# Performance work log

Hardware: AMD Instinct MI355X
Metric: run time of the kernel (lower is better)

## Reference

```python
import jax, jax.numpy as jnp
import numpy as np

THRESH = 0.999  # dynamic outlier percentile

# Standard NF4 signpost values (normalized to [-1, 1])
NF4 = np.array([-1.0, -0.6961928009986877, -0.5250730514526367, -0.39491748809814453,
                -0.28444138169288635, -0.18477343022823334, -0.09105003625154495, 0.0,
                0.07958029955625534, 0.16093020141124725, 0.24611230194568634, 0.33791524171829224,
                0.44070982933044434, 0.5626170039176941, 0.7229568362236023, 1.0], dtype=np.float32)


def setup_inputs() -> dict:
    key = jax.random.key(0)
    k1, k2 = jax.random.split(key)
    x = jax.random.normal(k1, (4096, 4096), dtype=jnp.float32)        # [tokens, in_features]
    weight = jax.random.normal(k2, (4096, 4096), dtype=jnp.float32)   # [out_features, in_features]
    nf_lut = jnp.asarray(NF4)                                          # [16] NF4 poles
    return {"x": x, "weight": weight, "nf_lut": nf_lut}


def quantize_nf(weight, nf_lut):
    # --- dynamic outlier detection (get_outliers_dynamic, qchannel=-1) ---
    t = 1.0 - (1.0 - THRESH) / 2.0
    upper = jnp.quantile(weight, t, axis=-1, keepdims=True)        # [R,1]
    lower = jnp.quantile(weight, 1.0 - t, axis=-1, keepdims=True)  # [R,1]
    outlier_mask = (weight <= lower) | (weight >= upper)           # [R,C] bool

    # --- include_sparse scale computation (quant_fn_nf) ---
    outliers0 = weight * outlier_mask
    median = jnp.median(weight, axis=-1, keepdims=True)
    tmp = weight - outliers0 + median * outlier_mask               # outliers replaced by median
    maxval = jnp.max(tmp, axis=-1, keepdims=True)
    minval = jnp.min(tmp, axis=-1, keepdims=True)
    offset = (maxval + minval) * 0.5
    rangeval = (maxval - minval) * 0.5

    w = weight - offset
    outliers = w * outlier_mask        # sparse (fp) component
    w = w - outliers                   # dense component
    w_scaled = w / rangeval            # normalized to ~[-1, 1]

    # --- nearest-pole (NF) rounding: argmin over |w - pole| ---
    idx = jnp.argmin(jnp.abs(w_scaled[..., None] - nf_lut), axis=-1)  # [R,C]
    Q = nf_lut[idx].astype(jnp.float16).astype(jnp.float32)           # .half() in torch

    # --- dequant ---
    qw = Q * rangeval + outliers + offset
    qw = jnp.nan_to_num(qw, nan=0.0, posinf=0.0, neginf=0.0)
    return qw


def reference(x, weight, nf_lut):
    qweight = quantize_nf(weight, nf_lut)   # simulated NF4 dense+sparse dequant
    return x @ qweight.T                    # [tokens, out_features]
```

## Files before the change

kernel.cpp:

```cpp
#include <hip/hip_runtime.h>
#include <hip/hip_fp16.h>
#include <stdint.h>

typedef __attribute__((ext_vector_type(4))) float f32x4;
typedef __attribute__((ext_vector_type(8))) short short8;

__device__ __forceinline__ unsigned short f2bf(float f) {
  unsigned int b = __float_as_uint(f);
  b = b + 0x7FFFu + ((b >> 16) & 1u);
  return (unsigned short)(b >> 16);
}

#define CE(a, b) { float _lo = fminf((a), (b)), _hi = fmaxf((a), (b)); (a) = _lo; (b) = _hi; }

__device__ __forceinline__ void merge8(float x[8]) {
  CE(x[0], x[4]); CE(x[1], x[5]); CE(x[2], x[6]); CE(x[3], x[7]);
  CE(x[2], x[4]); CE(x[3], x[5]);
  CE(x[1], x[2]); CE(x[3], x[4]); CE(x[5], x[6]);
}

__global__ __launch_bounds__(256) void prep_kernel(const float* __restrict__ x,
                                                   const float* __restrict__ W,
                                                   const float* __restrict__ lut,
                                                   unsigned short* __restrict__ xb,
                                                   unsigned short* __restrict__ qb) {
  const int tid = threadIdx.x;

  if (blockIdx.x >= 4096) {
    int b = blockIdx.x - 4096;
    int base = b * 1024 + tid;
#pragma unroll
    for (int it = 0; it < 4; ++it) {
      int i = base + it * 256;
      f32x4 v = ((const f32x4*)x)[i];
      ushort4 u;
      u.x = f2bf(v[0]); u.y = f2bf(v[1]); u.z = f2bf(v[2]); u.w = f2bf(v[3]);
      ((ushort4*)xb)[i] = u;
    }
    return;
  }

  const int C = 4096;
  const int row = blockIdx.x;
  const int lane = tid & 63;
  const int wv = tid >> 6;

  __shared__ float s_luth[16];
  __shared__ float s_mid[15];
  __shared__ float s_red[4][8];
  __shared__ float s_par[4];

  if (tid < 16) {
    float f = lut[tid];
    s_luth[tid] = __half2float(__float2half(f));
  }
  if (tid < 15) s_mid[tid] = 0.5f * (lut[tid] + lut[tid + 1]);

  const f32x4* Wp = (const f32x4*)(W + (size_t)row * C);
  f32x4 v[4];
#pragma unroll
  for (int i = 0; i < 4; ++i) v[i] = Wp[i * 256 + tid];

  float bot[4] = {__builtin_inff(), __builtin_inff(), __builtin_inff(), __builtin_inff()};
  float top[4] = {-__builtin_inff(), -__builtin_inff(), -__builtin_inff(), -__builtin_inff()};
#pragma unroll
  for (int i = 0; i < 4; ++i) {
#pragma unroll
    for (int j = 0; j < 4; ++j) {
      float f = v[i][j];
      bot[3] = fminf(bot[3], f); CE(bot[2], bot[3]); CE(bot[1], bot[2]); CE(bot[0], bot[1]);
      top[0] = fmaxf(top[0], f); CE(top[0], top[1]); CE(top[1], top[2]); CE(top[2], top[3]);
    }
  }

#pragma unroll
  for (int d = 1; d < 64; d <<= 1) {
    float xx[8];
#pragma unroll
    for (int j = 0; j < 4; ++j) { xx[j] = bot[j]; xx[4 + j] = __shfl_xor(bot[j], d); }
    merge8(xx);
#pragma unroll
    for (int j = 0; j < 4; ++j) bot[j] = xx[j];
#pragma unroll
    for (int j = 0; j < 4; ++j) { xx[j] = top[j]; xx[4 + j] = __shfl_xor(top[j], d); }
    merge8(xx);
#pragma unroll
    for (int j = 0; j < 4; ++j) top[j] = xx[4 + j];
  }

  if (lane == 0) {
#pragma unroll
    for (int j = 0; j < 4; ++j) { s_red[wv][j] = bot[j]; s_red[wv][4 + j] = top[j]; }
  }
  __syncthreads();

  if (tid == 0) {
    float a[8], b[8], m[8];
#pragma unroll
    for (int j = 0; j < 4; ++j) { a[j] = s_red[0][j]; a[4 + j] = s_red[1][j]; }
    merge8(a);
#pragma unroll
    for (int j = 0; j < 4; ++j) { b[j] = s_red[2][j]; b[4 + j] = s_red[3][j]; }
    merge8(b);
#pragma unroll
    for (int j = 0; j < 4; ++j) { m[j] = a[j]; m[4 + j] = b[j]; }
    merge8(m);
    float lower = m[2] + 0.0475f * (m[3] - m[2]);
#pragma unroll
    for (int j = 0; j < 4; ++j) { a[j] = s_red[0][4 + j]; a[4 + j] = s_red[1][4 + j]; }
    merge8(a);
#pragma unroll
    for (int j = 0; j < 4; ++j) { b[j] = s_red[2][4 + j]; b[4 + j] = s_red[3][4 + j]; }
    merge8(b);
#pragma unroll
    for (int j = 0; j < 4; ++j) { m[j] = a[4 + j]; m[4 + j] = b[4 + j]; }
    merge8(m);
    float upper = m[4] + 0.9525f * (m[5] - m[4]);
    s_par[0] = lower; s_par[1] = upper;
  }
  __syncthreads();

  float lower = s_par[0], upper = s_par[1];

  float mn = __builtin_inff(), mx = -__builtin_inff();
#pragma unroll
  for (int i = 0; i < 4; ++i) {
#pragma unroll
    for (int j = 0; j < 4; ++j) {
      float f = v[i][j];
      bool outl = (f <= lower) || (f >= upper);
      if (!outl) { mn = fminf(mn, f); mx = fmaxf(mx, f); }
    }
  }
#pragma unroll
  for (int d = 1; d < 64; d <<= 1) {
    mn = fminf(mn, __shfl_xor(mn, d));
    mx = fmaxf(mx, __shfl_xor(mx, d));
  }
  if (lane == 0) { s_red[wv][0] = mn; s_red[wv][1] = mx; }
  __syncthreads();
  if (tid == 0) {
    float tmn = fminf(fminf(s_red[0][0], s_red[1][0]), fminf(s_red[2][0], s_red[3][0]));
    float tmx = fmaxf(fmaxf(s_red[0][1], s_red[1][1]), fmaxf(s_red[2][1], s_red[3][1]));
    s_par[2] = (tmx + tmn) * 0.5f;
    s_par[3] = (tmx - tmn) * 0.5f;
  }
  __syncthreads();
  float offset = s_par[2], range = s_par[3];
  float invr = 1.0f / range;

  unsigned short* outr = qb + (size_t)row * C;
#pragma unroll
  for (int i = 0; i < 4; ++i) {
    ushort4 o;
    unsigned short os[4];
#pragma unroll
    for (int j = 0; j < 4; ++j) {
      float f = v[i][j];
      bool outl = (f <= lower) || (f >= upper);
      float q;
      if (outl) {
        q = f;
      } else {
        float ws = (f - offset) * invr;
        int bi = (ws > s_mid[7]) ? 8 : 0;
        bi += (ws > s_mid[bi + 3]) ? 4 : 0;
        bi += (ws > s_mid[bi + 1]) ? 2 : 0;
        bi += (ws > s_mid[bi]) ? 1 : 0;
        q = s_luth[bi] * range + offset;
      }
      if (!isfinite(q)) q = 0.0f;
      os[j] = f2bf(q);
    }
    o.x = os[0]; o.y = os[1]; o.z = os[2]; o.w = os[3];
    ((ushort4*)outr)[i * 256 + tid] = o;
  }
}

#define GK 4096

__device__ __forceinline__ void gload16(const void* gp, void* lp) {
  __builtin_amdgcn_global_load_lds(
      (const __attribute__((address_space(1))) unsigned int*)(uintptr_t)gp,
      (__attribute__((address_space(3))) unsigned int*)(unsigned int)(uintptr_t)lp,
      16, 0, 0);
}

#define BAR()    __builtin_amdgcn_s_barrier()
#define LGKM0()  asm volatile("s_waitcnt lgkmcnt(0)" ::: "memory")
#define VM6()    asm volatile("s_waitcnt vmcnt(6)" ::: "memory")
#define PRIO1()  __builtin_amdgcn_s_setprio(1)
#define PRIO0()  __builtin_amdgcn_s_setprio(0)

__global__ __launch_bounds__(512, 2) void gemm_bt(const unsigned short* __restrict__ A,
                                                  const unsigned short* __restrict__ B,
                                                  float* __restrict__ C) {
  __shared__ __align__(16) unsigned short sA[2][2][8192];
  __shared__ __align__(16) unsigned short sB[2][2][8192];

  const int tid = threadIdx.x;
  const int lane = tid & 63;
  const int wv = tid >> 6;
  const int wm = wv >> 2, wn = wv & 3;
  const int fr = lane & 15, fk = lane >> 4;

  int bi = blockIdx.x;
  int swz = (bi & 7) * 32 + (bi >> 3);
  int brow = swz >> 4, bcol = swz & 15;

  const unsigned short* Abase = A + (size_t)brow * 256 * GK;
  const unsigned short* Bbase = B + (size_t)bcol * 256 * GK;

  const int cA = (fk * 16) ^ ((fr & 8) << 2);

  const int srow = (wv >> 1) * 16 + (lane >> 2);
  const int skelt = ((wv & 1) * 64 + (((lane & 3) * 16) ^ ((lane & 32) ? 32 : 0))) >> 1;

  auto stage = [&](const unsigned short* gb, unsigned short* lb, int h, int kt) {
    const unsigned short* g = gb + ((size_t)h * 128) * GK + kt * 64 + skelt;
    char* lc = (char*)lb + wv * 1024 + lane * 16;
#pragma unroll
    for (int l = 0; l < 2; ++l)
      gload16(g + (size_t)(l * 64 + srow) * GK, lc + l * 8192);
  };

  f32x4 acc[8][4];
#pragma unroll
  for (int m = 0; m < 8; ++m)
#pragma unroll
    for (int n = 0; n < 4; ++n) acc[m][n] = (f32x4){0.f, 0.f, 0.f, 0.f};

  stage(Abase, &sA[0][0][0], 0, 0);
  stage(Abase, &sA[0][1][0], 1, 0);
  stage(Bbase, &sB[0][0][0], 0, 0);
  stage(Bbase, &sB[0][1][0], 1, 0);
  stage(Bbase, &sB[1][0][0], 0, 1);
  stage(Bbase, &sB[1][1][0], 1, 1);
  stage(Abase, &sA[1][0][0], 0, 1);
  VM6();
  BAR();

  const int nsub = (wn & 1) * 4;

#pragma unroll 1
  for (int i = 0; i < 32; ++i) {
    const int ktA1 = 2 * i + 1;
    const int ktN0 = (2 * i + 2 < 64) ? 2 * i + 2 : 63;
    const int ktN1 = (2 * i + 3 < 64) ? 2 * i + 3 : 63;

    short8 af[4][2], bf0[2][2], bf1[2][2];

    {
      const char* bA = (const char*)&sA[0][wm][0];
      const char* bB = (const char*)&sB[0][wn >> 1][0];

#pragma unroll
      for (int m = 0; m < 4; ++m)
#pragma unroll
        for (int kh = 0; kh < 2; ++kh)
          af[m][kh] = *(const short8*)(bA + m * 2048 + kh * 1024 + fr * 64 + cA);
#pragma unroll
      for (int n = 0; n < 2; ++n)
#pragma unroll
        for (int kh = 0; kh < 2; ++kh)
          bf0[n][kh] = *(const short8*)(bB + (nsub + n) * 2048 + kh * 1024 + fr * 64 + cA);
      stage(Abase, &sA[1][1][0], 1, ktA1);
      BAR(); LGKM0(); PRIO1();
#pragma unroll
      for (int m = 0; m < 4; ++m)
#pragma unroll
        for (int n = 0; n < 2; ++n)
#pragma unroll
          for (int kh = 0; kh < 2; ++kh)
            acc[m][n] = __builtin_amdgcn_mfma_f32_16x16x32_bf16(af[m][kh], bf0[n][kh], acc[m][n], 0, 0, 0);
      PRIO0(); BAR();

#pragma unroll
      for (int n = 0; n < 2; ++n)
#pragma unroll
        for (int kh = 0; kh < 2; ++kh)
          bf1[n][kh] = *(const short8*)(bB + (nsub + n + 2) * 2048 + kh * 1024 + fr * 64 + cA);
      BAR(); LGKM0(); PRIO1();
#pragma unroll
      for (int m = 0; m < 4; ++m)
#pragma unroll
        for (int n = 0; n < 2; ++n)
#pragma unroll
          for (int kh = 0; kh < 2; ++kh)
            acc[m][n + 2] = __builtin_amdgcn_mfma_f32_16x16x32_bf16(af[m][kh], bf1[n][kh], acc[m][n + 2], 0, 0, 0);
      PRIO0(); BAR();

#pragma unroll
      for (int m = 0; m < 4; ++m)
#pragma unroll
        for (int kh = 0; kh < 2; ++kh)
          af[m][kh] = *(const short8*)(bA + (m + 4) * 2048 + kh * 1024 + fr * 64 + cA);
      stage(Bbase, &sB[0][0][0], 0, ktN0);
      BAR(); LGKM0(); PRIO1();
#pragma unroll
      for (int m = 0; m < 4; ++m)
#pragma unroll
        for (int n = 0; n < 2; ++n)
#pragma unroll
          for (int kh = 0; kh < 2; ++kh)
            acc[m + 4][n + 2] = __builtin_amdgcn_mfma_f32_16x16x32_bf16(af[m][kh], bf1[n][kh], acc[m + 4][n + 2], 0, 0, 0);
      PRIO0(); BAR();

      stage(Bbase, &sB[0][1][0], 1, ktN0);
      stage(Abase, &sA[0][0][0], 0, ktN0);
      BAR(); PRIO1();
#pragma unroll
      for (int m = 0; m < 4; ++m)
#pragma unroll
        for (int n = 0; n < 2; ++n)
#pragma unroll
          for (int kh = 0; kh < 2; ++kh)
            acc[m + 4][n] = __builtin_amdgcn_mfma_f32_16x16x32_bf16(af[m][kh], bf0[n][kh], acc[m + 4][n], 0, 0, 0);
      PRIO0();
      VM6(); BAR();
    }

    {
      const char* bA = (const char*)&sA[1][wm][0];
      const char* bB = (const char*)&sB[1][wn >> 1][0];

#pragma unroll
      for (int m = 0; m < 4; ++m)
#pragma unroll
        for (int kh = 0; kh < 2; ++kh)
          af[m][kh] = *(const short8*)(bA + m * 2048 + kh * 1024 + fr * 64 + cA);
#pragma unroll
      for (int n = 0; n < 2; ++n)
#pragma unroll
        for (int kh = 0; kh < 2; ++kh)
          bf0[n][kh] = *(const short8*)(bB + (nsub + n) * 2048 + kh * 1024 + fr * 64 + cA);
      stage(Abase, &sA[0][1][0], 1, ktN0);
      BAR(); LGKM0(); PRIO1();
#pragma unroll
      for (int m = 0; m < 4; ++m)
#pragma unroll
        for (int n = 0; n < 2; ++n)
#pragma unroll
          for (int kh = 0; kh < 2; ++kh)
            acc[m][n] = __builtin_amdgcn_mfma_f32_16x16x32_bf16(af[m][kh], bf0[n][kh], acc[m][n], 0, 0, 0);
      PRIO0(); BAR();

#pragma unroll
      for (int n = 0; n < 2; ++n)
#pragma unroll
        for (int kh = 0; kh < 2; ++kh)
          bf1[n][kh] = *(const short8*)(bB + (nsub + n + 2) * 2048 + kh * 1024 + fr * 64 + cA);
      BAR(); LGKM0(); PRIO1();
#pragma unroll
      for (int m = 0; m < 4; ++m)
#pragma unroll
        for (int n = 0; n < 2; ++n)
#pragma unroll
          for (int kh = 0; kh < 2; ++kh)
            acc[m][n + 2] = __builtin_amdgcn_mfma_f32_16x16x32_bf16(af[m][kh], bf1[n][kh], acc[m][n + 2], 0, 0, 0);
      PRIO0(); BAR();

#pragma unroll
      for (int m = 0; m < 4; ++m)
#pragma unroll
        for (int kh = 0; kh < 2; ++kh)
          af[m][kh] = *(const short8*)(bA + (m + 4) * 2048 + kh * 1024 + fr * 64 + cA);
      stage(Bbase, &sB[1][0][0], 0, ktN1);
      BAR(); LGKM0(); PRIO1();
#pragma unroll
      for (int m = 0; m < 4; ++m)
#pragma unroll
        for (int n = 0; n < 2; ++n)
#pragma unroll
          for (int kh = 0; kh < 2; ++kh)
            acc[m + 4][n + 2] = __builtin_amdgcn_mfma_f32_16x16x32_bf16(af[m][kh], bf1[n][kh], acc[m + 4][n + 2], 0, 0, 0);
      PRIO0(); BAR();

      stage(Bbase, &sB[1][1][0], 1, ktN1);
      stage(Abase, &sA[1][0][0], 0, ktN1);
      BAR(); PRIO1();
#pragma unroll
      for (int m = 0; m < 4; ++m)
#pragma unroll
        for (int n = 0; n < 2; ++n)
#pragma unroll
          for (int kh = 0; kh < 2; ++kh)
            acc[m + 4][n] = __builtin_amdgcn_mfma_f32_16x16x32_bf16(af[m][kh], bf0[n][kh], acc[m + 4][n], 0, 0, 0);
      PRIO0();
      VM6(); BAR();
    }
  }

  const int rbase = brow * 256 + wm * 128;
  const int cbase = bcol * 256 + wn * 64;
#pragma unroll
  for (int m = 0; m < 8; ++m)
#pragma unroll
    for (int n = 0; n < 4; ++n)
#pragma unroll
      for (int j = 0; j < 4; ++j) {
        int rr = rbase + m * 16 + fk * 4 + j;
        int cc = cbase + n * 16 + fr;
        C[(size_t)rr * GK + cc] = acc[m][n][j];
      }
}

extern "C" void kernel_launch(void* const* d_in, const int* in_sizes, int n_in,
                              void* d_out, int out_size, void* d_ws, size_t ws_size,
                              hipStream_t stream) {
  const float* x = (const float*)d_in[0];
  const float* W = (const float*)d_in[1];
  const float* lut = (const float*)d_in[2];
  float* out = (float*)d_out;

  unsigned short* xb = (unsigned short*)d_ws;
  unsigned short* qb = xb + (size_t)4096 * 4096;

  prep_kernel<<<8192, 256, 0, stream>>>(x, W, lut, xb, qb);
  gemm_bt<<<256, 512, 0, stream>>>(xb, qb, out);
}
```

Baseline: 155.9 us.

## Restructure GEMM main loop into per-tile double buffer with register prefetch

Replaces the hand-interleaved 8-phase loop, which had many barriers and explicit lgkmcnt waits, with a simpler per-K-tile loop. Each iteration runs all MFMAs, barriers once, issues global->LDS loads for tile t+2, waits on vmcnt(8), then preloads the next tile's A-low and B fragments into registers. The aim is fewer barriers and better overlap of LDS reads with MFMA. The trade-off is more live fragment registers and coarser overlap of global loads, since the loads are issued only after compute and the vmcnt wait is placed right after them.

```diff
diff --git a/kernel.cpp b/kernel.cpp
--- a/kernel.cpp
+++ b/kernel.cpp
@@ -187,8 +187,7 @@
 }
 
 #define BAR()    __builtin_amdgcn_s_barrier()
-#define LGKM0()  asm volatile("s_waitcnt lgkmcnt(0)" ::: "memory")
-#define VM6()    asm volatile("s_waitcnt vmcnt(6)" ::: "memory")
+#define VM8()    asm volatile("s_waitcnt vmcnt(8)" ::: "memory")
 #define PRIO1()  __builtin_amdgcn_s_setprio(1)
 #define PRIO0()  __builtin_amdgcn_s_setprio(0)
 
@@ -230,165 +229,108 @@
 #pragma unroll
     for (int n = 0; n < 4; ++n) acc[m][n] = (f32x4){0.f, 0.f, 0.f, 0.f};
 
+  const int nsub = (wn & 1) * 4;
+
   stage(Abase, &sA[0][0][0], 0, 0);
   stage(Abase, &sA[0][1][0], 1, 0);
   stage(Bbase, &sB[0][0][0], 0, 0);
   stage(Bbase, &sB[0][1][0], 1, 0);
+  stage(Abase, &sA[1][0][0], 0, 1);
+  stage(Abase, &sA[1][1][0], 1, 1);
   stage(Bbase, &sB[1][0][0], 0, 1);
   stage(Bbase, &sB[1][1][0], 1, 1);
-  stage(Abase, &sA[1][0][0], 0, 1);
-  VM6();
+  VM8();
   BAR();
 
-  const int nsub = (wn & 1) * 4;
+  short8 afL[4][2], afH[4][2], bf0[2][2], bf1[2][2];
+
+  {
+    const char* bA = (const char*)&sA[0][wm][0];
+    const char* bB = (const char*)&sB[0][wn >> 1][0];
+#pragma unroll
+    for (int m = 0; m < 4; ++m)
+#pragma unroll
+      for (int kh = 0; kh < 2; ++kh)
+        afL[m][kh] = *(const short8*)(bA + m * 2048 + kh * 1024 + fr * 64 + cA);
+#pragma unroll
+    for (int n = 0; n < 2; ++n)
+#pragma unroll
+      for (int kh = 0; kh < 2; ++kh) {
+        bf0[n][kh] = *(const short8*)(bB + (nsub + n) * 2048 + kh * 1024 + fr * 64 + cA);
+        bf1[n][kh] = *(const short8*)(bB + (nsub + n + 2) * 2048 + kh * 1024 + fr * 64 + cA);
+      }
+  }
 
 #pragma unroll 1
-  for (int i = 0; i < 32; ++i) {
-    const int ktA1 = 2 * i + 1;
-    const int ktN0 = (2 * i + 2 < 64) ? 2 * i + 2 : 63;
-    const int ktN1 = (2 * i + 3 < 64) ? 2 * i + 3 : 63;
-
-    short8 af[4][2], bf0[2][2], bf1[2][2];
-
-    {
-      const char* bA = (const char*)&sA[0][wm][0];
-      const char* bB = (const char*)&sB[0][wn >> 1][0];
-
-#pragma unroll
-      for (int m = 0; m < 4; ++m)
+  for (int t = 0; t < 64; ++t) {
+    const int c = t & 1;
+    const char* bA = (const char*)&sA[c][wm][0];
+    const char* bAn = (const char*)&sA[c ^ 1][wm][0];
+    const char* bBn = (const char*)&sB[c ^ 1][wn >> 1][0];
+
+    PRIO1();
+#pragma unroll
+    for (int m = 0; m < 4; ++m)
+#pragma unroll
+      for (int n = 0; n < 2; ++n)
 #pragma unroll
         for (int kh = 0; kh < 2; ++kh)
-          af[m][kh] = *(const short8*)(bA + m * 2048 + kh * 1024 + fr * 64 + cA);
+          acc[m][n] = __builtin_amdgcn_mfma_f32_16x16x32_bf16(afL[m][kh], bf0[n][kh], acc[m][n], 0, 0, 0);
+#pragma unroll
+    for (int m = 0; m < 4; ++m)
 #pragma unroll
       for (int n = 0; n < 2; ++n)
 #pragma unroll
         for (int kh = 0; kh < 2; ++kh)
-          bf0[n][kh] = *(const short8*)(bB + (nsub + n) * 2048 + kh * 1024 + fr * 64 + cA);
-      stage(Abase, &sA[1][1][0], 1, ktA1);
-      BAR(); LGKM0(); PRIO1();
-#pragma unroll
-      for (int m = 0; m < 4; ++m)
-#pragma unroll
-        for (int n = 0; n < 2; ++n)
-#pragma unroll
-          for (int kh = 0; kh < 2; ++kh)
-            acc[m][n] = __builtin_amdgcn_mfma_f32_16x16x32_bf16(af[m][kh], bf0[n][kh], acc[m][n], 0, 0, 0);
-      PRIO0(); BAR();
-
+          acc[m][n + 2] = __builtin_amdgcn_mfma_f32_16x16x32_bf16(afL[m][kh], bf1[n][kh], acc[m][n + 2], 0, 0, 0);
+    PRIO0();
+
+#pragma unroll
+    for (int m = 0; m < 4; ++m)
+#pragma unroll
+      for (int kh = 0; kh < 2; ++kh)
+        afH[m][kh] = *(const short8*)(bA + (m + 4) * 2048 + kh * 1024 + fr * 64 + cA);
+
+    PRIO1();
+#pragma unroll
+    for (int m = 0; m < 4; ++m)
 #pragma unroll
       for (int n = 0; n < 2; ++n)
 #pragma unroll
         for (int kh = 0; kh < 2; ++kh)
-          bf1[n][kh] = *(const short8*)(bB + (nsub + n + 2) * 2048 + kh * 1024 + fr * 64 + cA);
-      BAR(); LGKM0(); PRIO1();
-#pragma unroll
-      for (int m = 0; m < 4; ++m)
-#pragma unroll
-        for (int n = 0; n < 2; ++n)
-#pragma unroll
-          for (int kh = 0; kh < 2; ++kh)
-            acc[m][n + 2] = __builtin_amdgcn_mfma_f32_16x16x32_bf16(af[m][kh], bf1[n][kh], acc[m][n + 2], 0, 0, 0);
-      PRIO0(); BAR();
-
-#pragma unroll
-      for (int m = 0; m < 4; ++m)
+          acc[m + 4][n + 2] = __builtin_amdgcn_mfma_f32_16x16x32_bf16(afH[m][kh], bf1[n][kh], acc[m + 4][n + 2], 0, 0, 0);
+#pragma unroll
+    for (int m = 0; m < 4; ++m)
+#pragma unroll
+      for (int n = 0; n < 2; ++n)
 #pragma unroll
         for (int kh = 0; kh < 2; ++kh)
-          af[m][kh] = *(const short8*)(bA + (m + 4) * 2048 + kh * 1024 + fr * 64 + cA);
-      stage(Bbase, &sB[0][0][0], 0, ktN0);
-      BAR(); LGKM0(); PRIO1();
-#pragma unroll
-      for (int m = 0; m < 4; ++m)
-#pragma unroll
-        for (int n = 0; n < 2; ++n)
-#pragma unroll
-          for (int kh = 0; kh < 2; ++kh)
-            acc[m + 4][n + 2] = __builtin_amdgcn_mfma_f32_16x16x32_bf16(af[m][kh], bf1[n][kh], acc[m + 4][n + 2], 0, 0, 0);
-      PRIO0(); BAR();
-
-      stage(Bbase, &sB[0][1][0], 1, ktN0);
-      stage(Abase, &sA[0][0][0], 0, ktN0);
-      BAR(); PRIO1();
-#pragma unroll
-      for (int m = 0; m < 4; ++m)
-#pragma unroll
-        for (int n = 0; n < 2; ++n)
-#pragma unroll
-          for (int kh = 0; kh < 2; ++kh)
-            acc[m + 4][n] = __builtin_amdgcn_mfma_f32_16x16x32_bf16(af[m][kh], bf0[n][kh], acc[m + 4][n], 0, 0, 0);
-      PRIO0();
-      VM6(); BAR();
-    }
-
-    {
-      const char* bA = (const char*)&sA[1][wm][0];
-      const char* bB = (const char*)&sB[1][wn >> 1][0];
-
-#pragma unroll
-      for (int m = 0; m < 4; ++m)
-#pragma unroll
-        for (int kh = 0; kh < 2; ++kh)
-          af[m][kh] = *(const short8*)(bA + m * 2048 + kh * 1024 + fr * 64 + cA);
-#pragma unroll
-      for (int n = 0; n < 2; ++n)
-#pragma unroll
-        for (int kh = 0; kh < 2; ++kh)
-          bf0[n][kh] = *(const short8*)(bB + (nsub + n) * 2048 + kh * 1024 + fr * 64 + cA);
-      stage(Abase, &sA[0][1][0], 1, ktN0);
-      BAR(); LGKM0(); PRIO1();
-#pragma unroll
-      for (int m = 0; m < 4; ++m)
-#pragma unroll
-        for (int n = 0; n < 2; ++n)
-#pragma unroll
-          for (int kh = 0; kh < 2; ++kh)
-            acc[m][n] = __builtin_amdgcn_mfma_f32_16x16x32_bf16(af[m][kh], bf0[n][kh], acc[m][n], 0, 0, 0);
-      PRIO0(); BAR();
-
-#pragma unroll
-      for (int n = 0; n < 2; ++n)
-#pragma unroll
-        for (int kh = 0; kh < 2; ++kh)
-          bf1[n][kh] = *(const short8*)(bB + (nsub + n + 2) * 2048 + kh * 1024 + fr * 64 + cA);
-      BAR(); LGKM0(); PRIO1();
-#pragma unroll
-      for (int m = 0; m < 4; ++m)
-#pragma unroll
-        for (int n = 0; n < 2; ++n)
-#pragma unroll
-          for (int kh = 0; kh < 2; ++kh)
-            acc[m][n + 2] = __builtin_amdgcn_mfma_f32_16x16x32_bf16(af[m][kh], bf1[n][kh], acc[m][n + 2], 0, 0, 0);
-      PRIO0(); BAR();
-
-#pragma unroll
-      for (int m = 0; m < 4; ++m)
-#pragma unroll
-        for (int kh = 0; kh < 2; ++kh)
-          af[m][kh] = *(const short8*)(bA + (m + 4) * 2048 + kh * 1024 + fr * 64 + cA);
-      stage(Bbase, &sB[1][0][0], 0, ktN1);
-      BAR(); LGKM0(); PRIO1();
-#pragma unroll
-      for (int m = 0; m < 4; ++m)
-#pragma unroll
-        for (int n = 0; n < 2; ++n)
-#pragma unroll
-          for (int kh = 0; kh < 2; ++kh)
-            acc[m + 4][n + 2] = __builtin_amdgcn_mfma_f32_16x16x32_bf16(af[m][kh], bf1[n][kh], acc[m + 4][n + 2], 0, 0, 0);
-      PRIO0(); BAR();
-
-      stage(Bbase, &sB[1][1][0], 1, ktN1);
-      stage(Abase, &sA[1][0][0], 0, ktN1);
-      BAR(); PRIO1();
-#pragma unroll
-      for (int m = 0; m < 4; ++m)
-#pragma unroll
-        for (int n = 0; n < 2; ++n)
-#pragma unroll
-          for (int kh = 0; kh < 2; ++kh)
-            acc[m + 4][n] = __builtin_amdgcn_mfma_f32_16x16x32_bf16(af[m][kh], bf0[n][kh], acc[m + 4][n], 0, 0, 0);
-      PRIO0();
-      VM6(); BAR();
-    }
+          acc[m + 4][n] = __builtin_amdgcn_mfma_f32_16x16x32_bf16(afH[m][kh], bf0[n][kh], acc[m + 4][n], 0, 0, 0);
+    PRIO0();
+
+    BAR();
+
+    const int ktn = (t + 2 < 64) ? t + 2 : 63;
+    stage(Abase, &sA[c][0][0], 0, ktn);
+    stage(Abase, &sA[c][1][0], 1, ktn);
+    stage(Bbase, &sB[c][0][0], 0, ktn);
+    stage(Bbase, &sB[c][1][0], 1, ktn);
+
+    VM8();
+    BAR();
+
+#pragma unroll
+    for (int m = 0; m < 4; ++m)
+#pragma unroll
+      for (int kh = 0; kh < 2; ++kh)
+        afL[m][kh] = *(const short8*)(bAn + m * 2048 + kh * 1024 + fr * 64 + cA);
+#pragma unroll
+    for (int n = 0; n < 2; ++n)
+#pragma unroll
+      for (int kh = 0; kh < 2; ++kh) {
+        bf0[n][kh] = *(const short8*)(bBn + (nsub + n) * 2048 + kh * 1024 + fr * 64 + cA);
+        bf1[n][kh] = *(const short8*)(bBn + (nsub + n + 2) * 2048 + kh * 1024 + fr * 64 + cA);
+      }
   }
 
   const int rbase = brow * 256 + wm * 128;
```

New measurement: 162.0 us. 3.9% more time.

## Software-pipeline LDS fragment reads one phase ahead of MFMA blocks

Applied to the files above, without the earlier changes.

Restructures the GEMM main loop so each phase loads the next phase's A/B fragments from shared memory while the current MFMA group runs. This replaces the explicit lgkmcnt(0) waits and some of the barriers. Global-to-LDS staging now uses vmcnt(2) waits placed after specific stages. The aim is to hide LDS read latency behind matrix ops. The cost is higher register pressure from double-buffered fragments, plus a risk of reading LDS buffers before their staged loads have landed.

```diff
diff --git a/kernel.cpp b/kernel.cpp
--- a/kernel.cpp
+++ b/kernel.cpp
@@ -187,10 +187,12 @@
 }
 
 #define BAR()    __builtin_amdgcn_s_barrier()
-#define LGKM0()  asm volatile("s_waitcnt lgkmcnt(0)" ::: "memory")
+#define VM2()    asm volatile("s_waitcnt vmcnt(2)" ::: "memory")
 #define VM6()    asm volatile("s_waitcnt vmcnt(6)" ::: "memory")
 #define PRIO1()  __builtin_amdgcn_s_setprio(1)
 #define PRIO0()  __builtin_amdgcn_s_setprio(0)
+
+#define ARD(buf, m, kh)  (*(const short8*)((buf) + (m) * 2048 + (kh) * 1024 + fr * 64 + cA))
 
 __global__ __launch_bounds__(512, 2) void gemm_bt(const unsigned short* __restrict__ A,
                                                   const unsigned short* __restrict__ B,
@@ -229,6 +231,8 @@
   for (int m = 0; m < 8; ++m)
 #pragma unroll
     for (int n = 0; n < 4; ++n) acc[m][n] = (f32x4){0.f, 0.f, 0.f, 0.f};
+
+  const int nsub = (wn & 1) * 4;
 
   stage(Abase, &sA[0][0][0], 0, 0);
   stage(Abase, &sA[0][1][0], 1, 0);
@@ -240,155 +244,162 @@
   VM6();
   BAR();
 
-  const int nsub = (wn & 1) * 4;
+  short8 afL0[4][2], afH0[4][2], bf00[2][2], bf10[2][2];
+  short8 afL1[4][2], afH1[4][2], bf01[2][2], bf11[2][2];
+
+  {
+    const char* bA0 = (const char*)&sA[0][wm][0];
+    const char* bB0 = (const char*)&sB[0][wn >> 1][0];
+#pragma unroll
+    for (int m = 0; m < 4; ++m)
+#pragma unroll
+      for (int kh = 0; kh < 2; ++kh) afL0[m][kh] = ARD(bA0, m, kh);
+#pragma unroll
+    for (int n = 0; n < 2; ++n)
+#pragma unroll
+      for (int kh = 0; kh < 2; ++kh) bf00[n][kh] = ARD(bB0, nsub + n, kh);
+  }
 
 #pragma unroll 1
   for (int i = 0; i < 32; ++i) {
-    const int ktA1 = 2 * i + 1;
+    const int kt1 = 2 * i + 1;
     const int ktN0 = (2 * i + 2 < 64) ? 2 * i + 2 : 63;
     const int ktN1 = (2 * i + 3 < 64) ? 2 * i + 3 : 63;
 
-    short8 af[4][2], bf0[2][2], bf1[2][2];
-
-    {
-      const char* bA = (const char*)&sA[0][wm][0];
-      const char* bB = (const char*)&sB[0][wn >> 1][0];
-
-#pragma unroll
-      for (int m = 0; m < 4; ++m)
-#pragma unroll
-        for (int kh = 0; kh < 2; ++kh)
-          af[m][kh] = *(const short8*)(bA + m * 2048 + kh * 1024 + fr * 64 + cA);
-#pragma unroll
-      for (int n = 0; n < 2; ++n)
-#pragma unroll
-        for (int kh = 0; kh < 2; ++kh)
-          bf0[n][kh] = *(const short8*)(bB + (nsub + n) * 2048 + kh * 1024 + fr * 64 + cA);
-      stage(Abase, &sA[1][1][0], 1, ktA1);
-      BAR(); LGKM0(); PRIO1();
-#pragma unroll
-      for (int m = 0; m < 4; ++m)
-#pragma unroll
-        for (int n = 0; n < 2; ++n)
-#pragma unroll
-          for (int kh = 0; kh < 2; ++kh)
-            acc[m][n] = __builtin_amdgcn_mfma_f32_16x16x32_bf16(af[m][kh], bf0[n][kh], acc[m][n], 0, 0, 0);
-      PRIO0(); BAR();
-
-#pragma unroll
-      for (int n = 0; n < 2; ++n)
-#pragma unroll
-        for (int kh = 0; kh < 2; ++kh)
-          bf1[n][kh] = *(const short8*)(bB + (nsub + n + 2) * 2048 + kh * 1024 + fr * 64 + cA);
-      BAR(); LGKM0(); PRIO1();
-#pragma unroll
-      for (int m = 0; m < 4; ++m)
-#pragma unroll
-        for (int n = 0; n < 2; ++n)
-#pragma unroll
-          for (int kh = 0; kh < 2; ++kh)
-            acc[m][n + 2] = __builtin_amdgcn_mfma_f32_16x16x32_bf16(af[m][kh], bf1[n][kh], acc[m][n + 2], 0, 0, 0);
-      PRIO0(); BAR();
-
-#pragma unroll
-      for (int m = 0; m < 4; ++m)
-#pragma unroll
-        for (int kh = 0; kh < 2; ++kh)
-          af[m][kh] = *(const short8*)(bA + (m + 4) * 2048 + kh * 1024 + fr * 64 + cA);
-      stage(Bbase, &sB[0][0][0], 0, ktN0);
-      BAR(); LGKM0(); PRIO1();
-#pragma unroll
-      for (int m = 0; m < 4; ++m)
-#pragma unroll
-        for (int n = 0; n < 2; ++n)
-#pragma unroll
-          for (int kh = 0; kh < 2; ++kh)
-            acc[m + 4][n + 2] = __builtin_amdgcn_mfma_f32_16x16x32_bf16(af[m][kh], bf1[n][kh], acc[m + 4][n + 2], 0, 0, 0);
-      PRIO0(); BAR();
-
-      stage(Bbase, &sB[0][1][0], 1, ktN0);
-      stage(Abase, &sA[0][0][0], 0, ktN0);
-      BAR(); PRIO1();
-#pragma unroll
-      for (int m = 0; m < 4; ++m)
-#pragma unroll
-        for (int n = 0; n < 2; ++n)
-#pragma unroll
-          for (int kh = 0; kh < 2; ++kh)
-            acc[m + 4][n] = __builtin_amdgcn_mfma_f32_16x16x32_bf16(af[m][kh], bf0[n][kh], acc[m + 4][n], 0, 0, 0);
-      PRIO0();
-      VM6(); BAR();
-    }
-
-    {
-      const char* bA = (const char*)&sA[1][wm][0];
-      const char* bB = (const char*)&sB[1][wn >> 1][0];
-
-#pragma unroll
-      for (int m = 0; m < 4; ++m)
-#pragma unroll
-        for (int kh = 0; kh < 2; ++kh)
-          af[m][kh] = *(const short8*)(bA + m * 2048 + kh * 1024 + fr * 64 + cA);
-#pragma unroll
-      for (int n = 0; n < 2; ++n)
-#pragma unroll
-        for (int kh = 0; kh < 2; ++kh)
-          bf0[n][kh] = *(const short8*)(bB + (nsub + n) * 2048 + kh * 1024 + fr * 64 + cA);
-      stage(Abase, &sA[0][1][0], 1, ktN0);
-      BAR(); LGKM0(); PRIO1();
-#pragma unroll
-      for (int m = 0; m < 4; ++m)
-#pragma unroll
-        for (int n = 0; n < 2; ++n)
-#pragma unroll
-          for (int kh = 0; kh < 2; ++kh)
-            acc[m][n] = __builtin_amdgcn_mfma_f32_16x16x32_bf16(af[m][kh], bf0[n][kh], acc[m][n], 0, 0, 0);
-      PRIO0(); BAR();
-
-#pragma unroll
-      for (int n = 0; n < 2; ++n)
-#pragma unroll
-        for (int kh = 0; kh < 2; ++kh)
-          bf1[n][kh] = *(const short8*)(bB + (nsub + n + 2) * 2048 + kh * 1024 + fr * 64 + cA);
-      BAR(); LGKM0(); PRIO1();
-#pragma unroll
-      for (int m = 0; m < 4; ++m)
-#pragma unroll
-        for (int n = 0; n < 2; ++n)
-#pragma unroll
-          for (int kh = 0; kh < 2; ++kh)
-            acc[m][n + 2] = __builtin_amdgcn_mfma_f32_16x16x32_bf16(af[m][kh], bf1[n][kh], acc[m][n + 2], 0, 0, 0);
-      PRIO0(); BAR();
-
-#pragma unroll
-      for (int m = 0; m < 4; ++m)
-#pragma unroll
-        for (int kh = 0; kh < 2; ++kh)
-          af[m][kh] = *(const short8*)(bA + (m + 4) * 2048 + kh * 1024 + fr * 64 + cA);
-      stage(Bbase, &sB[1][0][0], 0, ktN1);
-      BAR(); LGKM0(); PRIO1();
-#pragma unroll
-      for (int m = 0; m < 4; ++m)
-#pragma unroll
-        for (int n = 0; n < 2; ++n)
-#pragma unroll
-          for (int kh = 0; kh < 2; ++kh)
-            acc[m + 4][n + 2] = __builtin_amdgcn_mfma_f32_16x16x32_bf16(af[m][kh], bf1[n][kh], acc[m + 4][n + 2], 0, 0, 0);
-      PRIO0(); BAR();
-
-      stage(Bbase, &sB[1][1][0], 1, ktN1);
-      stage(Abase, &sA[1][0][0], 0, ktN1);
-      BAR(); PRIO1();
-#pragma unroll
-      for (int m = 0; m < 4; ++m)
-#pragma unroll
-        for (int n = 0; n < 2; ++n)
-#pragma unroll
-          for (int kh = 0; kh < 2; ++kh)
-            acc[m + 4][n] = __builtin_amdgcn_mfma_f32_16x16x32_bf16(af[m][kh], bf0[n][kh], acc[m + 4][n], 0, 0, 0);
-      PRIO0();
-      VM6(); BAR();
-    }
+    const char* bA0 = (const char*)&sA[0][wm][0];
+    const char* bB0 = (const char*)&sB[0][wn >> 1][0];
+    const char* bA1 = (const char*)&sA[1][wm][0];
+    const char* bB1 = (const char*)&sB[1][wn >> 1][0];
+
+#pragma unroll
+    for (int n = 0; n < 2; ++n)
+#pragma unroll
+      for (int kh = 0; kh < 2; ++kh) bf10[n][kh] = ARD(bB0, nsub + n + 2, kh);
+    PRIO1();
+#pragma unroll
+    for (int m = 0; m < 4; ++m)
+#pragma unroll
+      for (int n = 0; n < 2; ++n)
+#pragma unroll
+        for (int kh = 0; kh < 2; ++kh)
+          acc[m][n] = __builtin_amdgcn_mfma_f32_16x16x32_bf16(afL0[m][kh], bf00[n][kh], acc[m][n], 0, 0, 0);
+    PRIO0();
+    stage(Abase, &sA[1][1][0], 1, kt1);
+    BAR();
+
+#pragma unroll
+    for (int m = 0; m < 4; ++m)
+#pragma unroll
+      for (int kh = 0; kh < 2; ++kh) afH0[m][kh] = ARD(bA0, m + 4, kh);
+    PRIO1();
+#pragma unroll
+    for (int m = 0; m < 4; ++m)
+#pragma unroll
+      for (int n = 0; n < 2; ++n)
+#pragma unroll
+        for (int kh = 0; kh < 2; ++kh)
+          acc[m][n + 2] = __builtin_amdgcn_mfma_f32_16x16x32_bf16(afL0[m][kh], bf10[n][kh], acc[m][n + 2], 0, 0, 0);
+    PRIO0();
+    BAR();
+
+    PRIO1();
+#pragma unroll
+    for (int m = 0; m < 4; ++m)
+#pragma unroll
+      for (int n = 0; n < 2; ++n)
+#pragma unroll
+        for (int kh = 0; kh < 2; ++kh)
+          acc[m + 4][n + 2] = __builtin_amdgcn_mfma_f32_16x16x32_bf16(afH0[m][kh], bf10[n][kh], acc[m + 4][n + 2], 0, 0, 0);
+    PRIO0();
+    stage(Bbase, &sB[0][0][0], 0, ktN0);
+    VM2();
+    BAR();
+
+#pragma unroll
+    for (int m = 0; m < 4; ++m)
+#pragma unroll
+      for (int kh = 0; kh < 2; ++kh) afL1[m][kh] = ARD(bA1, m, kh);
+#pragma unroll
+    for (int n = 0; n < 2; ++n)
+#pragma unroll
+      for (int kh = 0; kh < 2; ++kh) bf01[n][kh] = ARD(bB1, nsub + n, kh);
+    PRIO1();
+#pragma unroll
+    for (int m = 0; m < 4; ++m)
+#pragma unroll
+      for (int n = 0; n < 2; ++n)
+#pragma unroll
+        for (int kh = 0; kh < 2; ++kh)
+          acc[m + 4][n] = __builtin_amdgcn_mfma_f32_16x16x32_bf16(afH0[m][kh], bf00[n][kh], acc[m + 4][n], 0, 0, 0);
+    PRIO0();
+    stage(Bbase, &sB[0][1][0], 1, ktN0);
+    stage(Abase, &sA[0][0][0], 0, ktN0);
+    BAR();
+
+#pragma unroll
+    for (int n = 0; n < 2; ++n)
+#pragma unroll
+      for (int kh = 0; kh < 2; ++kh) bf11[n][kh] = ARD(bB1, nsub + n + 2, kh);
+    PRIO1();
+#pragma unroll
+    for (int m = 0; m < 4; ++m)
+#pragma unroll
+      for (int n = 0; n < 2; ++n)
+#pragma unroll
+        for (int kh = 0; kh < 2; ++kh)
+          acc[m][n] = __builtin_amdgcn_mfma_f32_16x16x32_bf16(afL1[m][kh], bf01[n][kh], acc[m][n], 0, 0, 0);
+    PRIO0();
+    stage(Abase, &sA[0][1][0], 1, ktN0);
+    BAR();
+
+#pragma unroll
+    for (int m = 0; m < 4; ++m)
+#pragma unroll
+      for (int kh = 0; kh < 2; ++kh) afH1[m][kh] = ARD(bA1, m + 4, kh);
+    PRIO1();
+#pragma unroll
+    for (int m = 0; m < 4; ++m)
+#pragma unroll
+      for (int n = 0; n < 2; ++n)
+#pragma unroll
+        for (int kh = 0; kh < 2; ++kh)
+          acc[m][n + 2] = __builtin_amdgcn_mfma_f32_16x16x32_bf16(afL1[m][kh], bf11[n][kh], acc[m][n + 2], 0, 0, 0);
+    PRIO0();
+    BAR();
+
+    PRIO1();
+#pragma unroll
+    for (int m = 0; m < 4; ++m)
+#pragma unroll
+      for (int n = 0; n < 2; ++n)
+#pragma unroll
+        for (int kh = 0; kh < 2; ++kh)
+          acc[m + 4][n + 2] = __builtin_amdgcn_mfma_f32_16x16x32_bf16(afH1[m][kh], bf11[n][kh], acc[m + 4][n + 2], 0, 0, 0);
+    PRIO0();
+    stage(Bbase, &sB[1][0][0], 0, ktN1);
+    VM2();
+    BAR();
+
+#pragma unroll
+    for (int m = 0; m < 4; ++m)
+#pragma unroll
+      for (int kh = 0; kh < 2; ++kh) afL0[m][kh] = ARD(bA0, m, kh);
+#pragma unroll
+    for (int n = 0; n < 2; ++n)
+#pragma unroll
+      for (int kh = 0; kh < 2; ++kh) bf00[n][kh] = ARD(bB0, nsub + n, kh);
+    PRIO1();
+#pragma unroll
+    for (int m = 0; m < 4; ++m)
+#pragma unroll
+      for (int n = 0; n < 2; ++n)
+#pragma unroll
+        for (int kh = 0; kh < 2; ++kh)
+          acc[m + 4][n] = __builtin_amdgcn_mfma_f32_16x16x32_bf16(afH1[m][kh], bf01[n][kh], acc[m + 4][n], 0, 0, 0);
+    PRIO0();
+    stage(Bbase, &sB[1][1][0], 1, ktN1);
+    stage(Abase, &sA[1][0][0], 0, ktN1);
+    BAR();
   }
 
   const int rbase = brow * 256 + wm * 128;
```

Result: faster. 151.1 us (median of 3 runs) (-3.1%).
